# Performance work log

Hardware: AMD Instinct MI355X
Metric: run time of the kernel (lower is better)

The kernel has to match this reference:

```python
import jax, jax.numpy as jnp
import numpy as np

BZ, C, H, W, M = 8, 64, 64, 64, 2048  # N = H*W = 4096 scene-graph nodes


def setup_inputs() -> dict:
    key = jax.random.key(0)
    k1, k2 = jax.random.split(key)
    sg_node_feats = jax.random.normal(k1, (BZ, C, H, W), dtype=jnp.float32)
    # weighted adjacency from SG nodes (N) to KG nodes (M)
    sg_kg_adj = jax.random.uniform(k2, (BZ, H * W, M), dtype=jnp.float32)
    return {"sg_node_feats": sg_node_feats, "sg_kg_adj": sg_kg_adj}


def reference(sg_node_feats, sg_kg_adj):
    bz, channels, height, width = sg_node_feats.shape
    x = sg_node_feats.reshape(bz, channels, height * width)  # (bz, C, N)
    degrees = sg_kg_adj.sum(axis=1)                          # (bz, M)
    norm = jnp.maximum(degrees, 1.0)                         # (bz, M)
    # broadcast-multiply + sum over N == batched GEMM (bz,C,N) x (bz,N,M)
    out = jnp.einsum('bcn,bnm->bcm', x, sg_kg_adj) / norm[:, None, :]
    return out.transpose(0, 2, 1)                            # (bz, M, C)
```

## Files before the change

kernel.cpp:

```cpp
#include <hip/hip_runtime.h>


typedef short bf16x8 __attribute__((ext_vector_type(8)));
typedef float f32x4 __attribute__((ext_vector_type(4)));

#define BZc 8
#define Cc 64
#define Nc 4096
#define Mc 2048
#define BMc 128
#define BKc 64
#define NSPLIT 4
#define NSEG (Nc / NSPLIT)
#define KITERS (NSEG / BKc)
#define SDW 36
#define PANEL (64 * SDW)

#define PSUM_ELEMS (BZc * Mc * Cc)
#define PDEG_ELEMS (BZc * Mc)

__device__ __forceinline__ unsigned int pkbf(float a, float b) {
  unsigned int ua = __float_as_uint(a) + 0x8000u;
  unsigned int ub = __float_as_uint(b) + 0x8000u;
  return (ua >> 16) | (ub & 0xffff0000u);
}

__global__ __launch_bounds__(512, 4) void sgkg_kernel(
    const float* __restrict__ x,
    const float* __restrict__ adj,
    float* __restrict__ ws)
{
  __shared__ unsigned int adjT[2 * PANEL];
  __shared__ float degs[BMc];

  const int t = threadIdx.x;
  const int l = t & 63;
  const int w = t >> 6;

  const int bz     = blockIdx.x >> 6;
  const int mb     = (blockIdx.x >> 2) & 15;
  const int kh     = blockIdx.x & 3;
  const int m_base = mb * BMc;

  const int mg  = ((w & 1) << 3) | (l & 7);
  const int p   = ((w >> 1) << 3) | (l >> 3);
  const int sm0 = mg << 2;

  const float* aptr =
      adj + (size_t)bz * Nc * Mc + (size_t)(kh * NSEG + 2 * p) * Mc + (m_base + sm0);
  const int wb = SDW * sm0 + (((p >> 2) ^ (mg & 7)) << 2) + (p & 3);

  const int m_off = (w & 3) << 5;
  const int c_b   = (w >> 2) << 5;
  const int l15   = l & 15;
  const int l4    = l >> 4;

  const float* xb =
      x + ((size_t)bz * Cc + (c_b + l15)) * Nc + kh * NSEG + (l4 << 3);

  int aaddr[2][2];
#pragma unroll
  for (int tm = 0; tm < 2; ++tm) {
    const int m  = m_off + tm * 16 + l15;
    const int q  = m >> 6;
    const int ml = m & 63;
    const int pi = (ml >> 2) & 7;
    aaddr[tm][0] = q * PANEL + SDW * ml + ((l4 ^ pi) << 2);
    aaddr[tm][1] = q * PANEL + SDW * ml + (((4 + l4) ^ pi) << 2);
  }

  if (t < BMc) degs[t] = 0.0f;

  f32x4 acc00 = {0.f,0.f,0.f,0.f}, acc01 = {0.f,0.f,0.f,0.f};
  f32x4 acc10 = {0.f,0.f,0.f,0.f}, acc11 = {0.f,0.f,0.f,0.f};
  float da00=0.f, da01=0.f, da02=0.f, da03=0.f;
  float da10=0.f, da11=0.f, da12=0.f, da13=0.f;

  float4 r00 = *(const float4*)(aptr);
  float4 r01 = *(const float4*)(aptr + Mc);
  float4 r10 = *(const float4*)(aptr + 64);
  float4 r11 = *(const float4*)(aptr + 64 + Mc);

  for (int it = 0; it < KITERS; ++it) {
    const float* xit0 = xb + it * BKc;
    const float* xit1 = xit0 + 16 * Nc;
    float4 x00 = *(const float4*)(xit0);
    float4 x01 = *(const float4*)(xit0 + 4);
    float4 x02 = *(const float4*)(xit0 + 32);
    float4 x03 = *(const float4*)(xit0 + 36);
    float4 x10 = *(const float4*)(xit1);
    float4 x11 = *(const float4*)(xit1 + 4);
    float4 x12 = *(const float4*)(xit1 + 32);
    float4 x13 = *(const float4*)(xit1 + 36);

    __syncthreads();

    adjT[wb          ]         = pkbf(r00.x, r01.x);
    adjT[wb +     SDW]         = pkbf(r00.y, r01.y);
    adjT[wb + 2 * SDW]         = pkbf(r00.z, r01.z);
    adjT[wb + 3 * SDW]         = pkbf(r00.w, r01.w);
    adjT[PANEL + wb          ] = pkbf(r10.x, r11.x);
    adjT[PANEL + wb +     SDW] = pkbf(r10.y, r11.y);
    adjT[PANEL + wb + 2 * SDW] = pkbf(r10.z, r11.z);
    adjT[PANEL + wb + 3 * SDW] = pkbf(r10.w, r11.w);

    da00 += r00.x + r01.x;  da01 += r00.y + r01.y;
    da02 += r00.z + r01.z;  da03 += r00.w + r01.w;
    da10 += r10.x + r11.x;  da11 += r10.y + r11.y;
    da12 += r10.z + r11.z;  da13 += r10.w + r11.w;

    const float* anext = (it + 1 < KITERS) ? (aptr + (size_t)BKc * Mc) : aptr;
    float4 s00 = *(const float4*)(anext);
    float4 s01 = *(const float4*)(anext + Mc);
    float4 s10 = *(const float4*)(anext + 64);
    float4 s11 = *(const float4*)(anext + 64 + Mc);

    union { uint4 u; bf16x8 v; } B00, B01, B10, B11;
    B00.u = make_uint4(pkbf(x00.x, x00.y), pkbf(x00.z, x00.w),
                       pkbf(x01.x, x01.y), pkbf(x01.z, x01.w));
    B01.u = make_uint4(pkbf(x02.x, x02.y), pkbf(x02.z, x02.w),
                       pkbf(x03.x, x03.y), pkbf(x03.z, x03.w));
    B10.u = make_uint4(pkbf(x10.x, x10.y), pkbf(x10.z, x10.w),
                       pkbf(x11.x, x11.y), pkbf(x11.z, x11.w));
    B11.u = make_uint4(pkbf(x12.x, x12.y), pkbf(x12.z, x12.w),
                       pkbf(x13.x, x13.y), pkbf(x13.z, x13.w));

    __syncthreads();

    bf16x8 a00 = *(const bf16x8*)(adjT + aaddr[0][0]);
    bf16x8 a10 = *(const bf16x8*)(adjT + aaddr[1][0]);
    acc00 = __builtin_amdgcn_mfma_f32_16x16x32_bf16(a00, B00.v, acc00, 0, 0, 0);
    acc01 = __builtin_amdgcn_mfma_f32_16x16x32_bf16(a00, B10.v, acc01, 0, 0, 0);
    acc10 = __builtin_amdgcn_mfma_f32_16x16x32_bf16(a10, B00.v, acc10, 0, 0, 0);
    acc11 = __builtin_amdgcn_mfma_f32_16x16x32_bf16(a10, B10.v, acc11, 0, 0, 0);
    bf16x8 a01 = *(const bf16x8*)(adjT + aaddr[0][1]);
    bf16x8 a11 = *(const bf16x8*)(adjT + aaddr[1][1]);
    acc00 = __builtin_amdgcn_mfma_f32_16x16x32_bf16(a01, B01.v, acc00, 0, 0, 0);
    acc01 = __builtin_amdgcn_mfma_f32_16x16x32_bf16(a01, B11.v, acc01, 0, 0, 0);
    acc10 = __builtin_amdgcn_mfma_f32_16x16x32_bf16(a11, B01.v, acc10, 0, 0, 0);
    acc11 = __builtin_amdgcn_mfma_f32_16x16x32_bf16(a11, B11.v, acc11, 0, 0, 0);

    aptr = anext;
    r00 = s00; r01 = s01; r10 = s10; r11 = s11;
  }

  __syncthreads();
  atomicAdd(&degs[     sm0 + 0], da00);
  atomicAdd(&degs[     sm0 + 1], da01);
  atomicAdd(&degs[     sm0 + 2], da02);
  atomicAdd(&degs[     sm0 + 3], da03);
  atomicAdd(&degs[64 + sm0 + 0], da10);
  atomicAdd(&degs[64 + sm0 + 1], da11);
  atomicAdd(&degs[64 + sm0 + 2], da12);
  atomicAdd(&degs[64 + sm0 + 3], da13);

  float* psum = ws + (size_t)kh * PSUM_ELEMS;
#pragma unroll
  for (int tm = 0; tm < 2; ++tm) {
#pragma unroll
    for (int ct = 0; ct < 2; ++ct) {
      const f32x4 acc = tm ? (ct ? acc11 : acc10) : (ct ? acc01 : acc00);
#pragma unroll
      for (int r = 0; r < 4; ++r) {
        const int ml   = m_off + tm * 16 + (l4 << 2) + r;
        const int c    = c_b + ct * 16 + l15;
        const size_t o = ((size_t)(bz * Mc + m_base + ml)) * Cc + c;
        psum[o] = acc[r];
      }
    }
  }

  __syncthreads();
  if (t < BMc) {
    float* pdeg = ws + (size_t)NSPLIT * PSUM_ELEMS + (size_t)kh * PDEG_ELEMS;
    pdeg[bz * Mc + m_base + t] = degs[t];
  }
}

__global__ __launch_bounds__(256) void norm_kernel(
    const float* __restrict__ ws, float* __restrict__ out)
{
  const int i = blockIdx.x * 256 + threadIdx.x;
  const float4* p0 = (const float4*)(ws);
  const float4* p1 = (const float4*)(ws + (size_t)1 * PSUM_ELEMS);
  const float4* p2 = (const float4*)(ws + (size_t)2 * PSUM_ELEMS);
  const float4* p3 = (const float4*)(ws + (size_t)3 * PSUM_ELEMS);
  const float* dg  = ws + (size_t)NSPLIT * PSUM_ELEMS;

  const int bm = i >> 4;
  const float den = fmaxf(dg[bm] + dg[PDEG_ELEMS + bm] +
                          dg[2 * PDEG_ELEMS + bm] + dg[3 * PDEG_ELEMS + bm], 1.0f);

  float4 a = p0[i];
  float4 b = p1[i];
  float4 c = p2[i];
  float4 d = p3[i];
  float4 r;
  r.x = (a.x + b.x + c.x + d.x) / den;
  r.y = (a.y + b.y + c.y + d.y) / den;
  r.z = (a.z + b.z + c.z + d.z) / den;
  r.w = (a.w + b.w + c.w + d.w) / den;
  ((float4*)out)[i] = r;
}

extern "C" void kernel_launch(void* const* d_in, const int* in_sizes, int n_in,
                              void* d_out, int out_size, void* d_ws, size_t ws_size,
                              hipStream_t stream) {
  const float* x   = (const float*)d_in[0];
  const float* adj = (const float*)d_in[1];
  float* out       = (float*)d_out;
  float* ws        = (float*)d_ws;
  (void)in_sizes; (void)n_in; (void)out_size; (void)ws_size;

  sgkg_kernel<<<dim3(BZc * (Mc / BMc) * NSPLIT), dim3(512), 0, stream>>>(x, adj, ws);
  norm_kernel<<<dim3(PSUM_ELEMS / 4 / 256), dim3(256), 0, stream>>>(ws, out);
}
```

Before: 378.8 us.

## Widen M tile to 256 and restructure warp-to-tile mapping for adj reuse

Doubles the M tile per block from 128 to 256, halving the grid. Each warp now loads 8 adjacency rows across a 256-wide stripe, writes them into four padded LDS panels, and computes 8 16x16 MFMA tiles over a 16-channel slice. This changes the load/compute split so each x fragment is reused across more M tiles and the LDS panel stride is padded to cut bank conflicts. The cost is more accumulator registers and LDS per block, lower occupancy (launch bound 2 instead of 4), and half as many blocks for latency hiding.

```diff
diff --git a/kernel.cpp b/kernel.cpp
--- a/kernel.cpp
+++ b/kernel.cpp
@@ -8,13 +8,14 @@
 #define Cc 64
 #define Nc 4096
 #define Mc 2048
-#define BMc 128
+#define BMc 256
 #define BKc 64
 #define NSPLIT 4
 #define NSEG (Nc / NSPLIT)
 #define KITERS (NSEG / BKc)
 #define SDW 36
-#define PANEL (64 * SDW)
+#define PSTRIDE (64 * SDW + 4)
+#define NPAN 4
 
 #define PSUM_ELEMS (BZc * Mc * Cc)
 #define PDEG_ELEMS (BZc * Mc)
@@ -25,148 +26,130 @@
   return (ua >> 16) | (ub & 0xffff0000u);
 }
 
-__global__ __launch_bounds__(512, 4) void sgkg_kernel(
+__global__ __launch_bounds__(512, 2) void sgkg_kernel(
     const float* __restrict__ x,
     const float* __restrict__ adj,
     float* __restrict__ ws)
 {
-  __shared__ unsigned int adjT[2 * PANEL];
+  __shared__ unsigned int adjT[NPAN * PSTRIDE];
   __shared__ float degs[BMc];
 
   const int t = threadIdx.x;
   const int l = t & 63;
   const int w = t >> 6;
 
-  const int bz     = blockIdx.x >> 6;
-  const int mb     = (blockIdx.x >> 2) & 15;
+  const int bz     = blockIdx.x >> 5;
+  const int mb     = (blockIdx.x >> 2) & 7;
   const int kh     = blockIdx.x & 3;
   const int m_base = mb * BMc;
 
-  const int mg  = ((w & 1) << 3) | (l & 7);
-  const int p   = ((w >> 1) << 3) | (l >> 3);
-  const int sm0 = mg << 2;
-
-  const float* aptr =
-      adj + (size_t)bz * Nc * Mc + (size_t)(kh * NSEG + 2 * p) * Mc + (m_base + sm0);
-  const int wb = SDW * sm0 + (((p >> 2) ^ (mg & 7)) << 2) + (p & 3);
-
-  const int m_off = (w & 3) << 5;
-  const int c_b   = (w >> 2) << 5;
-  const int l15   = l & 15;
-  const int l4    = l >> 4;
+  const int q   = l >> 4;
+  const int sm0 = (l & 15) << 2;
+  const int pi  = l & 7;
+  const int lm0 = l << 2;
+
+  const float* ap =
+      adj + ((size_t)bz * Nc + kh * NSEG + 8 * w) * Mc + (m_base + lm0);
+  const int wbase = q * PSTRIDE + SDW * sm0 + ((w ^ pi) << 2);
+
+  const int mh  = w >> 2;
+  const int cq  = w & 3;
+  const int c_b = cq << 4;
+  const int l15 = l & 15;
+  const int l4  = l >> 4;
 
   const float* xb =
       x + ((size_t)bz * Cc + (c_b + l15)) * Nc + kh * NSEG + (l4 << 3);
 
-  int aaddr[2][2];
-#pragma unroll
-  for (int tm = 0; tm < 2; ++tm) {
-    const int m  = m_off + tm * 16 + l15;
-    const int q  = m >> 6;
-    const int ml = m & 63;
-    const int pi = (ml >> 2) & 7;
-    aaddr[tm][0] = q * PANEL + SDW * ml + ((l4 ^ pi) << 2);
-    aaddr[tm][1] = q * PANEL + SDW * ml + (((4 + l4) ^ pi) << 2);
+  int abase[4][2];
+#pragma unroll
+  for (int k = 0; k < 4; ++k) {
+    const int ml = k * 16 + l15;
+    const int pr = (ml >> 2) & 7;
+    abase[k][0] = SDW * ml + ((l4 ^ pr) << 2);
+    abase[k][1] = SDW * ml + (((4 + l4) ^ pr) << 2);
   }
 
   if (t < BMc) degs[t] = 0.0f;
 
-  f32x4 acc00 = {0.f,0.f,0.f,0.f}, acc01 = {0.f,0.f,0.f,0.f};
-  f32x4 acc10 = {0.f,0.f,0.f,0.f}, acc11 = {0.f,0.f,0.f,0.f};
-  float da00=0.f, da01=0.f, da02=0.f, da03=0.f;
-  float da10=0.f, da11=0.f, da12=0.f, da13=0.f;
-
-  float4 r00 = *(const float4*)(aptr);
-  float4 r01 = *(const float4*)(aptr + Mc);
-  float4 r10 = *(const float4*)(aptr + 64);
-  float4 r11 = *(const float4*)(aptr + 64 + Mc);
+  f32x4 acc[8];
+#pragma unroll
+  for (int i = 0; i < 8; ++i) acc[i] = (f32x4){0.f, 0.f, 0.f, 0.f};
+  float dacc0 = 0.f, dacc1 = 0.f, dacc2 = 0.f, dacc3 = 0.f;
+
+  float4 R0[4], R1[4], S0[4], S1[4];
+#pragma unroll
+  for (int j = 0; j < 4; ++j) {
+    const float* pj = ap + (size_t)(2 * j) * Mc;
+    R0[j] = *(const float4*)pj;
+    R1[j] = *(const float4*)(pj + Mc);
+  }
 
   for (int it = 0; it < KITERS; ++it) {
-    const float* xit0 = xb + it * BKc;
-    const float* xit1 = xit0 + 16 * Nc;
-    float4 x00 = *(const float4*)(xit0);
-    float4 x01 = *(const float4*)(xit0 + 4);
-    float4 x02 = *(const float4*)(xit0 + 32);
-    float4 x03 = *(const float4*)(xit0 + 36);
-    float4 x10 = *(const float4*)(xit1);
-    float4 x11 = *(const float4*)(xit1 + 4);
-    float4 x12 = *(const float4*)(xit1 + 32);
-    float4 x13 = *(const float4*)(xit1 + 36);
+    const float* xit = xb + it * BKc;
+    float4 xa = *(const float4*)(xit);
+    float4 xbv = *(const float4*)(xit + 4);
+    float4 xc = *(const float4*)(xit + 32);
+    float4 xd = *(const float4*)(xit + 36);
 
     __syncthreads();
 
-    adjT[wb          ]         = pkbf(r00.x, r01.x);
-    adjT[wb +     SDW]         = pkbf(r00.y, r01.y);
-    adjT[wb + 2 * SDW]         = pkbf(r00.z, r01.z);
-    adjT[wb + 3 * SDW]         = pkbf(r00.w, r01.w);
-    adjT[PANEL + wb          ] = pkbf(r10.x, r11.x);
-    adjT[PANEL + wb +     SDW] = pkbf(r10.y, r11.y);
-    adjT[PANEL + wb + 2 * SDW] = pkbf(r10.z, r11.z);
-    adjT[PANEL + wb + 3 * SDW] = pkbf(r10.w, r11.w);
-
-    da00 += r00.x + r01.x;  da01 += r00.y + r01.y;
-    da02 += r00.z + r01.z;  da03 += r00.w + r01.w;
-    da10 += r10.x + r11.x;  da11 += r10.y + r11.y;
-    da12 += r10.z + r11.z;  da13 += r10.w + r11.w;
-
-    const float* anext = (it + 1 < KITERS) ? (aptr + (size_t)BKc * Mc) : aptr;
-    float4 s00 = *(const float4*)(anext);
-    float4 s01 = *(const float4*)(anext + Mc);
-    float4 s10 = *(const float4*)(anext + 64);
-    float4 s11 = *(const float4*)(anext + 64 + Mc);
-
-    union { uint4 u; bf16x8 v; } B00, B01, B10, B11;
-    B00.u = make_uint4(pkbf(x00.x, x00.y), pkbf(x00.z, x00.w),
-                       pkbf(x01.x, x01.y), pkbf(x01.z, x01.w));
-    B01.u = make_uint4(pkbf(x02.x, x02.y), pkbf(x02.z, x02.w),
-                       pkbf(x03.x, x03.y), pkbf(x03.z, x03.w));
-    B10.u = make_uint4(pkbf(x10.x, x10.y), pkbf(x10.z, x10.w),
-                       pkbf(x11.x, x11.y), pkbf(x11.z, x11.w));
-    B11.u = make_uint4(pkbf(x12.x, x12.y), pkbf(x12.z, x12.w),
-                       pkbf(x13.x, x13.y), pkbf(x13.z, x13.w));
+#pragma unroll
+    for (int j = 0; j < 4; ++j) {
+      const int wj = wbase + j;
+      adjT[wj          ] = pkbf(R0[j].x, R1[j].x);
+      adjT[wj +     SDW] = pkbf(R0[j].y, R1[j].y);
+      adjT[wj + 2 * SDW] = pkbf(R0[j].z, R1[j].z);
+      adjT[wj + 3 * SDW] = pkbf(R0[j].w, R1[j].w);
+      dacc0 += R0[j].x + R1[j].x;
+      dacc1 += R0[j].y + R1[j].y;
+      dacc2 += R0[j].z + R1[j].z;
+      dacc3 += R0[j].w + R1[j].w;
+    }
+
+    const int itn = (it + 1 < KITERS) ? (it + 1) : it;
+#pragma unroll
+    for (int j = 0; j < 4; ++j) {
+      const float* pj = ap + (size_t)(itn * BKc + 2 * j) * Mc;
+      S0[j] = *(const float4*)pj;
+      S1[j] = *(const float4*)(pj + Mc);
+    }
+
+    union { uint4 u; bf16x8 v; } B0, B1;
+    B0.u = make_uint4(pkbf(xa.x, xa.y), pkbf(xa.z, xa.w),
+                      pkbf(xbv.x, xbv.y), pkbf(xbv.z, xbv.w));
+    B1.u = make_uint4(pkbf(xc.x, xc.y), pkbf(xc.z, xc.w),
+                      pkbf(xd.x, xd.y), pkbf(xd.z, xd.w));
 
     __syncthreads();
 
-    bf16x8 a00 = *(const bf16x8*)(adjT + aaddr[0][0]);
-    bf16x8 a10 = *(const bf16x8*)(adjT + aaddr[1][0]);
-    acc00 = __builtin_amdgcn_mfma_f32_16x16x32_bf16(a00, B00.v, acc00, 0, 0, 0);
-    acc01 = __builtin_amdgcn_mfma_f32_16x16x32_bf16(a00, B10.v, acc01, 0, 0, 0);
-    acc10 = __builtin_amdgcn_mfma_f32_16x16x32_bf16(a10, B00.v, acc10, 0, 0, 0);
-    acc11 = __builtin_amdgcn_mfma_f32_16x16x32_bf16(a10, B10.v, acc11, 0, 0, 0);
-    bf16x8 a01 = *(const bf16x8*)(adjT + aaddr[0][1]);
-    bf16x8 a11 = *(const bf16x8*)(adjT + aaddr[1][1]);
-    acc00 = __builtin_amdgcn_mfma_f32_16x16x32_bf16(a01, B01.v, acc00, 0, 0, 0);
-    acc01 = __builtin_amdgcn_mfma_f32_16x16x32_bf16(a01, B11.v, acc01, 0, 0, 0);
-    acc10 = __builtin_amdgcn_mfma_f32_16x16x32_bf16(a11, B01.v, acc10, 0, 0, 0);
-    acc11 = __builtin_amdgcn_mfma_f32_16x16x32_bf16(a11, B11.v, acc11, 0, 0, 0);
-
-    aptr = anext;
-    r00 = s00; r01 = s01; r10 = s10; r11 = s11;
+#pragma unroll
+    for (int tm = 0; tm < 8; ++tm) {
+      const int qo = ((mh << 1) + (tm >> 2)) * PSTRIDE;
+      bf16x8 a0 = *(const bf16x8*)(adjT + qo + abase[tm & 3][0]);
+      acc[tm] = __builtin_amdgcn_mfma_f32_16x16x32_bf16(a0, B0.v, acc[tm], 0, 0, 0);
+      bf16x8 a1 = *(const bf16x8*)(adjT + qo + abase[tm & 3][1]);
+      acc[tm] = __builtin_amdgcn_mfma_f32_16x16x32_bf16(a1, B1.v, acc[tm], 0, 0, 0);
+    }
+
+#pragma unroll
+    for (int j = 0; j < 4; ++j) { R0[j] = S0[j]; R1[j] = S1[j]; }
   }
 
   __syncthreads();
-  atomicAdd(&degs[     sm0 + 0], da00);
-  atomicAdd(&degs[     sm0 + 1], da01);
-  atomicAdd(&degs[     sm0 + 2], da02);
-  atomicAdd(&degs[     sm0 + 3], da03);
-  atomicAdd(&degs[64 + sm0 + 0], da10);
-  atomicAdd(&degs[64 + sm0 + 1], da11);
-  atomicAdd(&degs[64 + sm0 + 2], da12);
-  atomicAdd(&degs[64 + sm0 + 3], da13);
+  atomicAdd(&degs[lm0 + 0], dacc0);
+  atomicAdd(&degs[lm0 + 1], dacc1);
+  atomicAdd(&degs[lm0 + 2], dacc2);
+  atomicAdd(&degs[lm0 + 3], dacc3);
 
   float* psum = ws + (size_t)kh * PSUM_ELEMS;
 #pragma unroll
-  for (int tm = 0; tm < 2; ++tm) {
-#pragma unroll
-    for (int ct = 0; ct < 2; ++ct) {
-      const f32x4 acc = tm ? (ct ? acc11 : acc10) : (ct ? acc01 : acc00);
-#pragma unroll
-      for (int r = 0; r < 4; ++r) {
-        const int ml   = m_off + tm * 16 + (l4 << 2) + r;
-        const int c    = c_b + ct * 16 + l15;
-        const size_t o = ((size_t)(bz * Mc + m_base + ml)) * Cc + c;
-        psum[o] = acc[r];
-      }
+  for (int tm = 0; tm < 8; ++tm) {
+#pragma unroll
+    for (int r = 0; r < 4; ++r) {
+      const int ml   = (mh << 7) + tm * 16 + (l4 << 2) + r;
+      const size_t o = ((size_t)(bz * Mc + m_base + ml)) * Cc + (c_b + l15);
+      psum[o] = acc[tm][r];
     }
   }
 
```

After: 365.5 us. 1.04x faster.
